# Kernel tuning notes

Measured on AMD Instinct MI355X. Metric: run time of the kernel, lower is better.

Reference implementation:

```python
import jax, jax.numpy as jnp
import numpy as np

L, B, N, D, H = 18, 2, 1024, 256, 4
DH = D // H  # head_dim = 64
LAYER_TYPES = ("self", "cross") * 9
BN_EPS = 1e-5


def setup_inputs() -> dict:
    key = jax.random.key(0)
    ks = jax.random.split(key, 8)
    s = 0.03  # small init scale keeps 18 residual layers numerically tame
    w = lambda k, shape: jax.random.normal(k, shape, jnp.float32) * s
    return dict(
        descriptors=jax.random.normal(ks[0], (B, 2, N, D), jnp.float32),
        mask=jnp.ones((B, 2, N), jnp.int32),
        qw=w(ks[1], (L, D, D)), qb=jnp.zeros((L, D), jnp.float32),
        kw=w(ks[2], (L, D, D)), kb=jnp.zeros((L, D), jnp.float32),
        vw=w(ks[3], (L, D, D)), vb=jnp.zeros((L, D), jnp.float32),
        ow=w(ks[4], (L, D, D)), ob=jnp.zeros((L, D), jnp.float32),
        w1=w(ks[5], (L, 2 * D, 2 * D)), b1=jnp.zeros((L, 2 * D), jnp.float32),
        bn_g=jnp.ones((L, 2 * D), jnp.float32), bn_b=jnp.zeros((L, 2 * D), jnp.float32),
        w2=w(ks[6], (L, 2 * D, D)), b2=jnp.zeros((L, D), jnp.float32),
    )


def _attention(x, src, m, i, qw, qb, kw, kb, vw, vb, ow, ob):
    b, n, d = x.shape
    q = (x @ qw[i] + qb[i]).reshape(b, n, H, DH)
    k = (src @ kw[i] + kb[i]).reshape(b, -1, H, DH)
    v = (src @ vw[i] + vb[i]).reshape(b, -1, H, DH)
    scores = jnp.einsum("bnhd,bmhd->bhnm", q, k) / (DH ** 0.5)
    scores = jnp.where(m[:, None, None, :] == 0, jnp.float32(-1e9), scores)
    probs = jax.nn.softmax(scores, axis=-1)  # fp32, matches torch dtype=float32
    out = jnp.einsum("bhnm,bmhd->bnhd", probs, v).reshape(b, n, d)
    return out @ ow[i] + ob[i]


def _propagate(x, src, m, i, qw, qb, kw, kb, vw, vb, ow, ob, w1, b1, bn_g, bn_b, w2, b2):
    a = _attention(x, src, m, i, qw, qb, kw, kb, vw, vb, ow, ob)
    h = jnp.concatenate([x, a], axis=-1)        # [B, N, 2D]
    h = h @ w1[i] + b1[i]                       # [B, N, 2D]
    # BatchNorm1d (training mode): per-channel stats over batch and keypoint dims
    mean = h.mean(axis=(0, 1))
    var = ((h - mean) ** 2).mean(axis=(0, 1))   # biased variance, as torch BN uses
    h = (h - mean) / jnp.sqrt(var + BN_EPS) * bn_g[i] + bn_b[i]
    h = jax.nn.relu(h)
    return h @ w2[i] + b2[i]                    # [B, N, D]


def reference(descriptors, mask, qw, qb, kw, kb, vw, vb, ow, ob, w1, b1, bn_g, bn_b, w2, b2):
    d0, d1 = descriptors[:, 0], descriptors[:, 1]
    m0, m1 = mask[:, 0], mask[:, 1]
    params = (qw, qb, kw, kb, vw, vb, ow, ob, w1, b1, bn_g, bn_b, w2, b2)
    for i, lt in enumerate(LAYER_TYPES):
        if lt == "cross":
            s0, s1, sm0, sm1 = d1, d0, m1, m0
        else:  # self
            s0, s1, sm0, sm1 = d0, d1, m0, m1
        delta0 = _propagate(d0, s0, sm0, i, *params)
        delta1 = _propagate(d1, s1, sm1, i, *params)
        d0 = d0 + delta0
        d1 = d1 + delta1
    return jnp.stack([d0, d1], axis=1)
```

## Files before the change

### kernel.cpp

```cpp
#include <hip/hip_runtime.h>


typedef __attribute__((ext_vector_type(8))) short bf16x8;
typedef __attribute__((ext_vector_type(4))) short bf16x4;
typedef __attribute__((ext_vector_type(4))) float floatx4;

__device__ __forceinline__ short f2b(float f) {
  unsigned u = __builtin_bit_cast(unsigned, f);
  unsigned r = (u + 0x7FFFu + ((u >> 16) & 1u)) >> 16;
  return (short)r;
}
__device__ __forceinline__ unsigned pack2(float a, float b) {
  return (unsigned)(unsigned short)f2b(a) | ((unsigned)(unsigned short)f2b(b) << 16);
}
__device__ __forceinline__ void split2(float a, float b, unsigned& h, unsigned& l) {
  unsigned short ha = (unsigned short)f2b(a), hb = (unsigned short)f2b(b);
  float fa = __builtin_bit_cast(float, (unsigned)ha << 16);
  float fb = __builtin_bit_cast(float, (unsigned)hb << 16);
  h = (unsigned)ha | ((unsigned)hb << 16);
  l = pack2(a - fa, b - fb);
}

__device__ __forceinline__ void gl2lds16(const void* g, void* l) {
  __builtin_amdgcn_global_load_lds(
      (const __attribute__((address_space(1))) unsigned*)g,
      (__attribute__((address_space(3))) unsigned*)l, 16, 0, 0);
}

__device__ __forceinline__ floatx4 mfma16_bf16(bf16x4 a, bf16x4 b, floatx4 c) {
#if __has_builtin(__builtin_amdgcn_mfma_f32_16x16x16_bf16)
  return __builtin_amdgcn_mfma_f32_16x16x16_bf16(a, b, c, 0, 0, 0);
#elif __has_builtin(__builtin_amdgcn_mfma_f32_16x16x16bf16_1k)
  return __builtin_amdgcn_mfma_f32_16x16x16bf16_1k(a, b, c, 0, 0, 0);
#else
  asm volatile("v_mfma_f32_16x16x16_bf16 %0, %1, %2, %0" : "+v"(c) : "v"(a), "v"(b));
  return c;
#endif
}

#define BARW   asm volatile("s_barrier" ::: "memory")
#define WAITV8 asm volatile("s_waitcnt vmcnt(8)" ::: "memory")
#define WAITV4 asm volatile("s_waitcnt vmcnt(4)" ::: "memory")
#define WAITV0 asm volatile("s_waitcnt vmcnt(0)" ::: "memory")
#define LGKM0  asm volatile("s_waitcnt lgkmcnt(0)" ::: "memory")
#define PRIO1  __builtin_amdgcn_s_setprio(1)
#define PRIO0  __builtin_amdgcn_s_setprio(0)

#define GEMM_IDS                                        \
  const int tid = threadIdx.x;                          \
  const int lane = tid & 63, w = tid >> 6;              \
  const int wy = w >> 1, wx = w & 1;                    \
  const int quad = lane >> 4, l16 = lane & 15;          \
  const int lr = lane >> 3;                             \
  const int lcs = (((lane & 7) ^ lr) & 7) * 8;          \
  const floatx4 z4 = {0.f, 0.f, 0.f, 0.f};

__device__ __forceinline__ void mfma_step_sw(const short* As, const short* Bs,
                                             int wy, int wx, int quad, int l16,
                                             floatx4 acc[2][4]) {
#pragma unroll
  for (int kk = 0; kk < 2; ++kk) {
    const int sw = (((kk * 4 + quad) ^ (l16 & 7)) * 8);
    bf16x8 a0 = *(const bf16x8*)&As[(wy * 32 + l16) * 64 + sw];
    bf16x8 a1 = *(const bf16x8*)&As[(wy * 32 + 16 + l16) * 64 + sw];
    bf16x8 b[4];
#pragma unroll
    for (int ni = 0; ni < 4; ++ni)
      b[ni] = *(const bf16x8*)&Bs[(wx * 64 + ni * 16 + l16) * 64 + sw];
#pragma unroll
    for (int ni = 0; ni < 4; ++ni) {
      acc[0][ni] = __builtin_amdgcn_mfma_f32_16x16x32_bf16(a0, b[ni], acc[0][ni], 0, 0, 0);
      acc[1][ni] = __builtin_amdgcn_mfma_f32_16x16x32_bf16(a1, b[ni], acc[1][ni], 0, 0, 0);
    }
  }
}

__device__ __forceinline__ void mfma_step_sw32(const short* As, const short* Bs,
                                               int wy, int wx, int quad, int l16,
                                               floatx4 acc[4]) {
#pragma unroll
  for (int kk = 0; kk < 2; ++kk) {
    const int sw = (((kk * 4 + quad) ^ (l16 & 7)) * 8);
    bf16x8 a0 = *(const bf16x8*)&As[(wy * 16 + l16) * 64 + sw];
    bf16x8 b[4];
#pragma unroll
    for (int ni = 0; ni < 4; ++ni)
      b[ni] = *(const bf16x8*)&Bs[(wx * 64 + ni * 16 + l16) * 64 + sw];
#pragma unroll
    for (int ni = 0; ni < 4; ++ni)
      acc[ni] = __builtin_amdgcn_mfma_f32_16x16x32_bf16(a0, b[ni], acc[ni], 0, 0, 0);
  }
}

__device__ __forceinline__ void mfma_step_sw32x64(const short* As, const short* Bs,
                                                  int wy, int wx, int quad, int l16,
                                                  floatx4 acc[2]) {
#pragma unroll
  for (int kk = 0; kk < 2; ++kk) {
    const int sw = (((kk * 4 + quad) ^ (l16 & 7)) * 8);
    bf16x8 a0 = *(const bf16x8*)&As[(wy * 16 + l16) * 64 + sw];
    bf16x8 b[2];
#pragma unroll
    for (int ni = 0; ni < 2; ++ni)
      b[ni] = *(const bf16x8*)&Bs[(wx * 32 + ni * 16 + l16) * 64 + sw];
#pragma unroll
    for (int ni = 0; ni < 2; ++ni)
      acc[ni] = __builtin_amdgcn_mfma_f32_16x16x32_bf16(a0, b[ni], acc[ni], 0, 0, 0);
  }
}

__global__ __launch_bounds__(256) void wfuse(
    const float* __restrict__ ow, const float* __restrict__ w1,
    short* __restrict__ wbuf) {
  __shared__ short As_h[64 * 64], As_l[64 * 64];
  __shared__ short Bs_h[128 * 64], Bs_l[128 * 64];
  const int blk = blockIdx.x;
  const int layer = blk >> 4, sub = blk & 15;
  const int kp0 = (sub & 3) * 64, n0 = (sub >> 2) * 128;
  const float* A = ow + (size_t)layer * 65536;
  const float* Bw = w1 + (size_t)layer * 262144 + 256 * 512;
  short* w1t = wbuf + (size_t)layer * 655360 + 262144;
  GEMM_IDS;
  (void)lr; (void)lcs;
  floatx4 acc[2][4] = {{z4, z4, z4, z4}, {z4, z4, z4, z4}};
  const int ar = tid >> 2, aq = tid & 3;
  const int bn = tid & 127, bkh = tid >> 7;

  for (int s = 0; s < 4; ++s) {
    const int k0 = s * 64;
    const float* Ar = &A[(size_t)(kp0 + ar) * 256 + k0 + aq * 16];
    float4 f0 = *(const float4*)&Ar[0];
    float4 f1 = *(const float4*)&Ar[4];
    float4 f2 = *(const float4*)&Ar[8];
    float4 f3 = *(const float4*)&Ar[12];
    float bv[32];
#pragma unroll
    for (int kk2 = 0; kk2 < 32; ++kk2)
      bv[kk2] = Bw[(size_t)(k0 + bkh * 32 + kk2) * 512 + n0 + bn];

    __syncthreads();
    {
      uint4 hi, lo;
      split2(f0.x, f0.y, hi.x, lo.x);
      split2(f0.z, f0.w, hi.y, lo.y);
      split2(f1.x, f1.y, hi.z, lo.z);
      split2(f1.z, f1.w, hi.w, lo.w);
      int sl = ((aq * 2) ^ (ar & 7)) * 8;
      *(uint4*)&As_h[ar * 64 + sl] = hi;
      *(uint4*)&As_l[ar * 64 + sl] = lo;
      split2(f2.x, f2.y, hi.x, lo.x);
      split2(f2.z, f2.w, hi.y, lo.y);
      split2(f3.x, f3.y, hi.z, lo.z);
      split2(f3.z, f3.w, hi.w, lo.w);
      sl = ((aq * 2 + 1) ^ (ar & 7)) * 8;
      *(uint4*)&As_h[ar * 64 + sl] = hi;
      *(uint4*)&As_l[ar * 64 + sl] = lo;
    }
#pragma unroll
    for (int cc = 0; cc < 4; ++cc) {
      uint4 hi, lo;
      split2(bv[cc * 8 + 0], bv[cc * 8 + 1], hi.x, lo.x);
      split2(bv[cc * 8 + 2], bv[cc * 8 + 3], hi.y, lo.y);
      split2(bv[cc * 8 + 4], bv[cc * 8 + 5], hi.z, lo.z);
      split2(bv[cc * 8 + 6], bv[cc * 8 + 7], hi.w, lo.w);
      int sl = ((bkh * 4 + cc) ^ (bn & 7)) * 8;
      *(uint4*)&Bs_h[bn * 64 + sl] = hi;
      *(uint4*)&Bs_l[bn * 64 + sl] = lo;
    }
    __syncthreads();
    mfma_step_sw(As_h, Bs_h, wy, wx, quad, l16, acc);
    mfma_step_sw(As_h, Bs_l, wy, wx, quad, l16, acc);
    mfma_step_sw(As_l, Bs_h, wy, wx, quad, l16, acc);
  }
#pragma unroll
  for (int mi = 0; mi < 2; ++mi)
#pragma unroll
    for (int ni = 0; ni < 4; ++ni) {
      int col = n0 + wx * 64 + ni * 16 + l16;
      int row0 = kp0 + wy * 32 + mi * 16 + quad * 4;
      uint2 uu;
      uu.x = pack2(acc[mi][ni][0], acc[mi][ni][1]);
      uu.y = pack2(acc[mi][ni][2], acc[mi][ni][3]);
      *(uint2*)&w1t[(size_t)col * 512 + 256 + row0] = uu;
    }
}

__global__ __launch_bounds__(256) void wprep(
    const float* __restrict__ qw, const float* __restrict__ kw,
    const float* __restrict__ vw, const float* __restrict__ w1,
    const float* __restrict__ w2, const float* __restrict__ ob,
    const float* __restrict__ b1, short* __restrict__ wbuf,
    float* __restrict__ beff, const float* __restrict__ desc,
    float* __restrict__ xd, short* __restrict__ xb,
    float* __restrict__ psz) {
  __shared__ float SH[32 * 130];
  int blk = blockIdx.x;
  int t = threadIdx.x;
  if (blk < 2592) {
    int layer = blk / 144;
    int sub2 = blk % 144;
    int sub = sub2 >> 1;
    int khalf = sub2 & 1;
    const float* W; int Kd, Nd, k0, n0; size_t ooff;
    if (sub < 24) {
      int wsel = sub / 8; int tt = sub & 7;
      k0 = (tt >> 1) * 64; n0 = (tt & 1) * 128; Kd = 256; Nd = 256;
      W = (wsel == 0 ? qw : wsel == 1 ? kw : vw) + (size_t)layer * 65536;
      ooff = (size_t)wsel * 65536;
    } else if (sub < 56) {
      int tt = sub - 24; k0 = (tt >> 2) * 64; n0 = (tt & 3) * 128;
      Kd = 512; Nd = 512; W = w1 + (size_t)layer * 262144; ooff = 262144;
    } else {
      int tt = sub - 56; k0 = (tt >> 1) * 64; n0 = (tt & 1) * 128;
      Kd = 512; Nd = 256; W = w2 + (size_t)layer * 131072; ooff = 524288;
    }
    k0 += khalf * 32;
    short* out = wbuf + (size_t)layer * 655360 + ooff;
    const int rr = t >> 4;
    const int c4 = (t & 15) * 4;
#pragma unroll
    for (int i = 0; i < 2; ++i)
#pragma unroll
      for (int hf = 0; hf < 2; ++hf) {
        float4 v = *(const float4*)&W[(size_t)(k0 + i * 16 + rr) * Nd + n0 + hf * 64 + c4];
        float* tp = &SH[(i * 16 + rr) * 130 + hf * 64 + c4];
        tp[0] = v.x; tp[1] = v.y; tp[2] = v.z; tp[3] = v.w;
      }
    __syncthreads();
    const int n = t >> 1;
    const int kh = (t & 1) * 16;
    float v[16];
#pragma unroll
    for (int kk = 0; kk < 16; ++kk)
      v[kk] = SH[(kh + kk) * 130 + n];
    unsigned u[8];
#pragma unroll
    for (int j2 = 0; j2 < 8; ++j2) u[j2] = pack2(v[2 * j2], v[2 * j2 + 1]);
    short* op = &out[(size_t)(n0 + n) * Kd + k0 + kh];
    uint4 o1; o1.x = u[0]; o1.y = u[1]; o1.z = u[2]; o1.w = u[3];
    uint4 o2; o2.x = u[4]; o2.y = u[5]; o2.z = u[6]; o2.w = u[7];
    *(uint4*)&op[0] = o1;
    *(uint4*)&op[8] = o2;
  } else if (blk < 2736) {
    int bb = blk - 2592;
    int layer = bb >> 3;
    int n0 = (bb & 7) * 64;
    const float* obL = ob + (size_t)layer * 256;
    const float* w1L = w1 + (size_t)layer * 262144 + 256 * 512;
    int n = n0 + (t & 63);
    int part = t >> 6;
    float s = 0.f;
    for (int i = part * 64; i < part * 64 + 64; ++i)
      s += obL[i] * w1L[(size_t)i * 512 + n];
    SH[part * 64 + (t & 63)] = s;
    __syncthreads();
    if (t < 64) {
      float tot = SH[t] + SH[64 + t] + SH[128 + t] + SH[192 + t] +
                  b1[(size_t)layer * 512 + n0 + t];
      beff[(size_t)layer * 512 + n0 + t] = tot;
    }
  } else if (blk < 3760) {
    int idx = (blk - 2736) * 256 + t;
    int fi = idx << 2;
    int hi = (fi >> 19) & 1;
    int lo = (fi >> 18) & 1;
    int sj = (fi & ~(3 << 18)) | (lo << 19) | (hi << 18);
    float4 v = *(const float4*)&desc[sj];
    *(float4*)&xd[fi] = v;
    uint2 uu; uu.x = pack2(v.x, v.y); uu.y = pack2(v.z, v.w);
    *(uint2*)&xb[fi] = uu;
  } else {
    int idx = (blk - 3760) * 1024 + t * 4;
    float4 zz = {0.f, 0.f, 0.f, 0.f};
    *(float4*)&psz[idx] = zz;
  }
}

__global__ __launch_bounds__(256, 2) void gemm_qkv(
    const short* __restrict__ xb, const short* __restrict__ wbufL,
    const float* __restrict__ qb_, const float* __restrict__ kb_,
    const float* __restrict__ vb_,
    short* __restrict__ q, short* __restrict__ kout, short* __restrict__ vT,
    int cross) {
  __shared__ short SM[40960];
  short* As = SM;
  short* Bs = SM + 8192;
  const int bid = blockIdx.x;
  const int swz = (bid & 7) * 96 + (bid >> 3);
  const int rb = (swz / 6) * 32;
  const int cb = (swz % 6) * 128;
  const int seg = cb >> 8;
  const int cbl = cb & 255;
  int arb = rb;
  if (seg) arb = (rb & 2047) | ((((rb >> 11) ^ cross) & 1) << 11);
  const short* A = xb + (size_t)arb * 256;
  const short* Wt = wbufL + (size_t)seg * 65536 + (size_t)cbl * 256;
  const float* bias = (seg == 0 ? qb_ : seg == 1 ? kb_ : vb_) + cbl;
  GEMM_IDS;
  floatx4 acc[4] = {z4, z4, z4, z4};

#pragma unroll
  for (int s = 0; s < 4; ++s) {
    const int k0 = s * 64;
    gl2lds16(&A[(size_t)(w * 8 + lr) * 256 + k0 + lcs], &As[s * 2048 + (w * 8) * 64]);
#pragma unroll
    for (int i = 0; i < 4; ++i)
      gl2lds16(&Wt[(size_t)(i * 32 + w * 8 + lr) * 256 + k0 + lcs],
               &Bs[s * 8192 + (i * 32 + w * 8) * 64]);
  }
  WAITV0;
  BARW;
#pragma unroll
  for (int s = 0; s < 4; ++s)
    mfma_step_sw32(&As[s * 2048], &Bs[s * 8192], wy, wx, quad, l16, acc);

  if (seg < 2) {
    short* C = (seg == 0 ? q : kout) + (size_t)rb * 256 + cbl;
#pragma unroll
    for (int ni = 0; ni < 4; ++ni) {
      int col = wx * 64 + ni * 16 + l16;
      float bc = bias[col];
#pragma unroll
      for (int reg = 0; reg < 4; ++reg) {
        int row = wy * 16 + quad * 4 + reg;
        C[(size_t)row * 256 + col] = f2b(acc[ni][reg] + bc);
      }
    }
  } else {
    BARW;
    short* T = SM + w * 1536;
    const int sb = rb >> 10;
    const int hh = (cbl >> 6) + wx;
    const int z = sb * 4 + hh;
#pragma unroll
    for (int ni = 0; ni < 4; ++ni) {
      int col = wx * 64 + ni * 16 + l16;
      float bc = bias[col];
#pragma unroll
      for (int reg = 0; reg < 4; ++reg)
        T[(ni * 16 + l16) * 24 + quad * 4 + reg] = f2b(acc[ni][reg] + bc);
    }
    short* dst = &vT[((size_t)z * 64 + lane) * 1024 + (rb & 1023) + wy * 16];
    *(uint4*)&dst[0] = *(const uint4*)&T[lane * 24 + 0];
    *(uint4*)&dst[8] = *(const uint4*)&T[lane * 24 + 8];
  }
}

__global__ __launch_bounds__(256, 3) void attn_mfma(
    const short* __restrict__ q, const short* __restrict__ k,
    const short* __restrict__ vT, const int* __restrict__ mask,
    short* __restrict__ attnb, int cross) {
  __shared__ short Ks[2][2][4096];
  __shared__ short Vs[2][4096];
  __shared__ float Msk[1024];
  const int tid = threadIdx.x;
  const int lane = tid & 63, w = tid >> 6;
  const int wv = w & 1, wq = w >> 1;
  const int quad = lane >> 4, l16 = lane & 15;
  const int lr = lane >> 3;
  const int lcs = (((lane & 7) ^ lr) & 7) * 8;
  const int bid = blockIdx.x;
  const int swz = (bid & 7) * 64 + (bid >> 3);
  const int qt = swz & 31;
  const int z = swz >> 5;
  const int sb = z >> 2, h = z & 3;
  const int s = sb >> 1, b = sb & 1;
  const int rowbase = sb * 1024;
  const int* mp = mask + (b * 2 + (s ^ cross)) * 1024;

  const int qrow = qt * 32 + wq * 16 + l16;
  bf16x8 qf[2];
#pragma unroll
  for (int kk = 0; kk < 2; ++kk)
    qf[kk] = *(const bf16x8*)&q[(size_t)(rowbase + qrow) * 256 + h * 64 + kk * 32 + quad * 8];

  {
    int4 mv = *(const int4*)&mp[tid * 4];
    Msk[tid * 4 + 0] = (mv.x == 0) ? -1.0e9f : 0.f;
    Msk[tid * 4 + 1] = (mv.y == 0) ? -1.0e9f : 0.f;
    Msk[tid * 4 + 2] = (mv.z == 0) ? -1.0e9f : 0.f;
    Msk[tid * 4 + 3] = (mv.w == 0) ? -1.0e9f : 0.f;
  }

  const floatx4 z4 = {0.f, 0.f, 0.f, 0.f};
  floatx4 o4[4] = {z4, z4, z4, z4};
  float mrun = -1e30f, lsum = 0.f;

#define ATT_STAGE_K(t, buf)                                                             \
  {                                                                                     \
    int key0s = wv * 512 + (t) * 64;                                                    \
    _Pragma("unroll") for (int j = 0; j < 4; ++j)                                       \
      gl2lds16(&k[(size_t)(rowbase + key0s + j * 16 + wq * 8 + lr) * 256 + h * 64 + lcs], \
               &Ks[buf][wv][(j * 16 + wq * 8) * 64]);                                   \
  }
#define ATT_STAGE_V(t)                                                                  \
  {                                                                                     \
    int key0s = wv * 512 + (t) * 64;                                                    \
    _Pragma("unroll") for (int j = 0; j < 4; ++j)                                       \
      gl2lds16(&vT[((size_t)z * 64 + j * 16 + wq * 8 + lr) * 1024 + key0s + lcs],       \
               &Vs[wv][(j * 16 + wq * 8) * 64]);                                        \
  }

  ATT_STAGE_K(0, 0);
  ATT_STAGE_V(0);
  __syncthreads();
  for (int t = 0; t < 8; ++t) {
    int buf = t & 1;
    if (t < 7) { ATT_STAGE_K(t + 1, buf ^ 1); WAITV8; } else { WAITV4; }
    BARW;
    const int key0 = wv * 512 + t * 64;

    floatx4 sA[4] = {z4, z4, z4, z4};
    PRIO1;
#pragma unroll
    for (int kk = 0; kk < 2; ++kk) {
      const int sw = (((kk * 4 + quad) ^ (l16 & 7)) * 8);
#pragma unroll
      for (int mt = 0; mt < 4; ++mt) {
        bf16x8 kf = *(const bf16x8*)&Ks[buf][wv][(mt * 16 + l16) * 64 + sw];
        sA[mt] = __builtin_amdgcn_mfma_f32_16x16x32_bf16(kf, qf[kk], sA[mt], 0, 0, 0);
      }
    }
    PRIO0;
    float scv[4][4];
    float tmax = -1e30f;
#pragma unroll
    for (int mt = 0; mt < 4; ++mt) {
      float4 mk = *(const float4*)&Msk[key0 + mt * 16 + quad * 4];
      scv[mt][0] = sA[mt][0] * 0.125f + mk.x;
      scv[mt][1] = sA[mt][1] * 0.125f + mk.y;
      scv[mt][2] = sA[mt][2] * 0.125f + mk.z;
      scv[mt][3] = sA[mt][3] * 0.125f + mk.w;
#pragma unroll
      for (int reg = 0; reg < 4; ++reg) tmax = fmaxf(tmax, scv[mt][reg]);
    }
    tmax = fmaxf(tmax, __shfl_xor(tmax, 16));
    tmax = fmaxf(tmax, __shfl_xor(tmax, 32));
    float mnew = fmaxf(mrun, tmax);
    float corr = __expf(mrun - mnew);
    mrun = mnew;
    lsum *= corr;
#pragma unroll
    for (int dt = 0; dt < 4; ++dt)
#pragma unroll
      for (int reg = 0; reg < 4; ++reg) o4[dt][reg] *= corr;

    bf16x4 pb[4];
#pragma unroll
    for (int mt = 0; mt < 4; ++mt) {
      float e0 = __expf(scv[mt][0] - mnew);
      float e1 = __expf(scv[mt][1] - mnew);
      float e2 = __expf(scv[mt][2] - mnew);
      float e3 = __expf(scv[mt][3] - mnew);
      lsum += (e0 + e1) + (e2 + e3);
      union { bf16x4 v; uint2 u; } pu;
      pu.u.x = pack2(e0, e1); pu.u.y = pack2(e2, e3);
      pb[mt] = pu.v;
    }
    if (t < 7) { WAITV4; } else { WAITV0; }
    BARW;
    PRIO1;
#pragma unroll
    for (int mt = 0; mt < 4; ++mt) {
      const int c2 = mt * 2 + (quad >> 1);
      const int sub = (quad & 1) * 4;
#pragma unroll
      for (int dt = 0; dt < 4; ++dt) {
        bf16x4 vf = *(const bf16x4*)&Vs[wv][(dt * 16 + l16) * 64 +
                                            ((c2 ^ (l16 & 7)) * 8) + sub];
        o4[dt] = mfma16_bf16(vf, pb[mt], o4[dt]);
      }
    }
    PRIO0;
    LGKM0;
    BARW;
    if (t < 7) ATT_STAGE_V(t + 1);
  }
  lsum += __shfl_xor(lsum, 16);
  lsum += __shfl_xor(lsum, 32);

  float* MG = (float*)&Ks[0][0][0];
  const int mo = (wq * 64 + lane) * 18;
  if (wv == 1) {
    MG[mo] = mrun;
    MG[mo + 1] = lsum;
#pragma unroll
    for (int dt = 0; dt < 4; ++dt)
#pragma unroll
      for (int reg = 0; reg < 4; ++reg) MG[mo + 2 + dt * 4 + reg] = o4[dt][reg];
  }
  __syncthreads();
  if (wv == 0) {
    float m2 = MG[mo], l2 = MG[mo + 1];
    float mm = fmaxf(mrun, m2);
    float ca = __expf(mrun - mm), cb2 = __expf(m2 - mm);
    float inv = 1.f / (ca * lsum + cb2 * l2);
    short* op = &attnb[(size_t)(rowbase + qrow) * 256 + h * 64 + quad * 4];
#pragma unroll
    for (int dt = 0; dt < 4; ++dt) {
      float v0 = (ca * o4[dt][0] + cb2 * MG[mo + 2 + dt * 4 + 0]) * inv;
      float v1 = (ca * o4[dt][1] + cb2 * MG[mo + 2 + dt * 4 + 1]) * inv;
      float v2 = (ca * o4[dt][2] + cb2 * MG[mo + 2 + dt * 4 + 2]) * inv;
      float v3 = (ca * o4[dt][3] + cb2 * MG[mo + 2 + dt * 4 + 3]) * inv;
      uint2 uu;
      uu.x = pack2(v0, v1);
      uu.y = pack2(v2, v3);
      *(uint2*)&op[dt * 16] = uu;
    }
  }
#undef ATT_STAGE_K
#undef ATT_STAGE_V
}

__global__ __launch_bounds__(256, 2) void gemm_w1(
    const short* __restrict__ xb, const short* __restrict__ attnb,
    const short* __restrict__ w1t, const float* __restrict__ beff,
    float* __restrict__ hbuf, float* __restrict__ psumL, float* __restrict__ psqL) {
  __shared__ short SM[40960];
  short* As = SM;
  short* Bs = SM + 8192;
  const int bid = blockIdx.x;
  const int swz = (bid & 7) * 64 + (bid >> 3);
  const int rb = (swz >> 2) * 32, cb = (swz & 3) * 128;
  const int str = rb >> 11;
  GEMM_IDS;
  floatx4 acc[4] = {z4, z4, z4, z4};

#pragma unroll
  for (int h = 0; h < 2; ++h) {
    if (h) BARW;
    const short* Ap = (h == 0 ? xb : attnb) + (size_t)rb * 256;
#pragma unroll
    for (int st = 0; st < 4; ++st) {
      const int k0 = h * 256 + st * 64;
      gl2lds16(&Ap[(size_t)(w * 8 + lr) * 256 + st * 64 + lcs],
               &As[st * 2048 + (w * 8) * 64]);
#pragma unroll
      for (int i = 0; i < 4; ++i)
        gl2lds16(&w1t[(size_t)(cb + i * 32 + w * 8 + lr) * 512 + k0 + lcs],
                 &Bs[st * 8192 + (i * 32 + w * 8) * 64]);
    }
    WAITV0;
    BARW;
#pragma unroll
    for (int st = 0; st < 4; ++st)
      mfma_step_sw32(&As[st * 2048], &Bs[st * 8192], wy, wx, quad, l16, acc);
  }

  float colsum[4], colsq[4];
#pragma unroll
  for (int ni = 0; ni < 4; ++ni) { colsum[ni] = 0.f; colsq[ni] = 0.f; }
#pragma unroll
  for (int ni = 0; ni < 4; ++ni) {
    int col = wx * 64 + ni * 16 + l16;
    float bc = beff[cb + col];
#pragma unroll
    for (int reg = 0; reg < 4; ++reg) {
      int row = rb + wy * 16 + quad * 4 + reg;
      float val = acc[ni][reg] + bc;
      hbuf[(size_t)row * 512 + cb + col] = val;
      colsum[ni] += val; colsq[ni] += val * val;
    }
  }
#pragma unroll
  for (int ni = 0; ni < 4; ++ni)
#pragma unroll
    for (int d = 16; d < 64; d <<= 1) {
      colsum[ni] += __shfl_xor(colsum[ni], d);
      colsq[ni]  += __shfl_xor(colsq[ni], d);
    }
  __syncthreads();
  float (*Ps)[2][128] = (float(*)[2][128])SM;
  if (quad == 0) {
#pragma unroll
    for (int ni = 0; ni < 4; ++ni) {
      Ps[wy][0][wx * 64 + ni * 16 + l16] = colsum[ni];
      Ps[wy][1][wx * 64 + ni * 16 + l16] = colsq[ni];
    }
  }
  __syncthreads();
  if (tid < 128) {
    atomicAdd(&psumL[str * 512 + cb + tid], Ps[0][0][tid] + Ps[1][0][tid]);
    atomicAdd(&psqL [str * 512 + cb + tid], Ps[0][1][tid] + Ps[1][1][tid]);
  }
}

__global__ __launch_bounds__(256, 3) void gemm_w2(
    const float* __restrict__ hbuf, const short* __restrict__ w2t,
    const float* __restrict__ b2_, const float* __restrict__ psumL,
    const float* __restrict__ psqL, const float* __restrict__ g,
    const float* __restrict__ be, float* __restrict__ xd, short* __restrict__ xb,
    float* __restrict__ outp) {
  __shared__ short SM[24576];
  __shared__ float s_scale[512], s_shift[512];
  short* As = SM;
  short* Bs = SM + 8192;
  const int bid = blockIdx.x;
  const int swz = (bid & 7) * 64 + (bid >> 3);
  const int rb = (swz >> 2) * 32, cb = (swz & 3) * 64;
  const int str = rb >> 11;
  GEMM_IDS;
  floatx4 acc[2] = {z4, z4};
#pragma unroll
  for (int cc = 0; cc < 2; ++cc) {
    int c = tid + cc * 256;
    float sum = psumL[str * 512 + c];
    float sq  = psqL [str * 512 + c];
    float mean = sum * (1.f / 2048.f);
    float var = sq * (1.f / 2048.f) - mean * mean;
    float rstd = rsqrtf(var + 1e-5f);
    float gs = g[c] * rstd;
    s_scale[c] = gs;
    s_shift[c] = be[c] - mean * gs;
  }
  __syncthreads();

  const int p = tid & 7, ar = tid >> 3;

#pragma unroll
  for (int h = 0; h < 2; ++h) {
    if (h) BARW;
#pragma unroll
    for (int st = 0; st < 4; ++st) {
      const int k0 = h * 256 + st * 64;
#pragma unroll
      for (int i = 0; i < 2; ++i)
        gl2lds16(&w2t[(size_t)(cb + i * 32 + w * 8 + lr) * 512 + k0 + lcs],
                 &Bs[st * 4096 + (i * 32 + w * 8) * 64]);
    }
#pragma unroll
    for (int st = 0; st < 4; ++st) {
      const int cs = h * 256 + st * 64 + ((p ^ (ar & 7)) * 8);
      float4 h0 = *(const float4*)&hbuf[(size_t)(rb + ar) * 512 + cs];
      float4 h1 = *(const float4*)&hbuf[(size_t)(rb + ar) * 512 + cs + 4];
      float4 sc0 = *(const float4*)&s_scale[cs];
      float4 sc1 = *(const float4*)&s_scale[cs + 4];
      float4 sh0 = *(const float4*)&s_shift[cs];
      float4 sh1 = *(const float4*)&s_shift[cs + 4];
      uint4 pk;
      pk.x = pack2(fmaxf(h0.x * sc0.x + sh0.x, 0.f), fmaxf(h0.y * sc0.y + sh0.y, 0.f));
      pk.y = pack2(fmaxf(h0.z * sc0.z + sh0.z, 0.f), fmaxf(h0.w * sc0.w + sh0.w, 0.f));
      pk.z = pack2(fmaxf(h1.x * sc1.x + sh1.x, 0.f), fmaxf(h1.y * sc1.y + sh1.y, 0.f));
      pk.w = pack2(fmaxf(h1.z * sc1.z + sh1.z, 0.f), fmaxf(h1.w * sc1.w + sh1.w, 0.f));
      *(uint4*)&As[st * 2048 + ar * 64 + p * 8] = pk;
    }
    WAITV0;
    LGKM0;
    BARW;
#pragma unroll
    for (int st = 0; st < 4; ++st)
      mfma_step_sw32x64(&As[st * 2048], &Bs[st * 4096], wy, wx, quad, l16, acc);
  }

#pragma unroll
  for (int ni = 0; ni < 2; ++ni) {
    int col = cb + wx * 32 + ni * 16 + l16;
    float bc = b2_[col];
#pragma unroll
    for (int reg = 0; reg < 4; ++reg) {
      int row = rb + wy * 16 + quad * 4 + reg;
      float r = xd[(size_t)row * 256 + col] + acc[ni][reg] + bc;
      xd[(size_t)row * 256 + col] = r;
      xb[(size_t)row * 256 + col] = f2b(r);
      if (outp) {
        int ss = row >> 11, bb = (row >> 10) & 1, n = row & 1023;
        outp[(size_t)((bb * 2 + ss) * 1024 + n) * 256 + col] = r;
      }
    }
  }
}

extern "C" void kernel_launch(void* const* d_in, const int* in_sizes, int n_in,
                              void* d_out, int out_size, void* d_ws, size_t ws_size,
                              hipStream_t stream) {
  (void)in_sizes; (void)n_in; (void)out_size; (void)ws_size;
  const float* desc = (const float*)d_in[0];
  const int*   mask = (const int*)d_in[1];
  const float* qw = (const float*)d_in[2];
  const float* qb = (const float*)d_in[3];
  const float* kw = (const float*)d_in[4];
  const float* kb = (const float*)d_in[5];
  const float* vw = (const float*)d_in[6];
  const float* vb = (const float*)d_in[7];
  const float* ow = (const float*)d_in[8];
  const float* ob = (const float*)d_in[9];
  const float* w1 = (const float*)d_in[10];
  const float* b1 = (const float*)d_in[11];
  const float* bn_g = (const float*)d_in[12];
  const float* bn_b = (const float*)d_in[13];
  const float* w2 = (const float*)d_in[14];
  const float* b2 = (const float*)d_in[15];
  float* out = (float*)d_out;

  char* base = (char*)d_ws;
  float* xd    = (float*)(base);
  float* hbuf  = (float*)(base + (4u << 20));
  short* xb    = (short*)(base + (12u << 20));
  short* qb16  = (short*)(base + (14u << 20));
  short* kb16  = (short*)(base + (16u << 20));
  short* vTb   = (short*)(base + (18u << 20));
  short* attnb = (short*)(base + (20u << 20));
  float* psum  = (float*)(base + (22u << 20));
  float* psq   = psum + 18 * 1024;
  float* beff  = psq + 18 * 1024;
  short* wbuf  = (short*)(base + (24u << 20));

  wprep<<<3796, 256, 0, stream>>>(qw, kw, vw, w1, w2, ob, b1,
                                  wbuf, beff, desc, xd, xb, psum);
  wfuse<<<288, 256, 0, stream>>>(ow, w1, wbuf);

  for (int i = 0; i < 18; ++i) {
    int cross = i & 1;
    short* wb = wbuf + (size_t)i * 655360;

    gemm_qkv<<<768, 256, 0, stream>>>(
        xb, wb, qb + (size_t)i * 256, kb + (size_t)i * 256, vb + (size_t)i * 256,
        qb16, kb16, vTb, cross);
    attn_mfma<<<512, 256, 0, stream>>>(qb16, kb16, vTb, mask, attnb, cross);
    gemm_w1<<<512, 256, 0, stream>>>(xb, attnb, wb + 262144,
                                     beff + (size_t)i * 512,
                                     hbuf, psum + (size_t)i * 1024,
                                     psq + (size_t)i * 1024);
    gemm_w2<<<512, 256, 0, stream>>>(hbuf, wb + 524288,
                                     b2 + (size_t)i * 256,
                                     psum + (size_t)i * 1024,
                                     psq + (size_t)i * 1024,
                                     bn_g + (size_t)i * 512,
                                     bn_b + (size_t)i * 512, xd, xb,
                                     (i == 17) ? out : nullptr);
  }
}
```

Before: 883.1 us.

## Double-buffer K-loop and double M-tile in QKV, W1, W2 GEMMs

The three projection GEMMs now use 64-row tiles instead of 32, halving the grid sizes. Each K loop changes from loading all stages and then computing into a two-buffer pipeline: global-to-LDS loads of stage s+2 (or s+1 in W2) are issued while stage s is multiplied. LDS use per block drops, so launch bounds rise to allow more resident blocks. The intent is to overlap memory latency with MFMA work and reuse each weight tile across more rows. The cost is fewer blocks on a GPU with many CUs, and extra barriers inside every K step.

```diff
diff --git a/kernel.cpp b/kernel.cpp
--- a/kernel.cpp
+++ b/kernel.cpp
@@ -40,6 +40,7 @@
 
 #define BARW   asm volatile("s_barrier" ::: "memory")
 #define WAITV8 asm volatile("s_waitcnt vmcnt(8)" ::: "memory")
+#define WAITV6 asm volatile("s_waitcnt vmcnt(6)" ::: "memory")
 #define WAITV4 asm volatile("s_waitcnt vmcnt(4)" ::: "memory")
 #define WAITV0 asm volatile("s_waitcnt vmcnt(0)" ::: "memory")
 #define LGKM0  asm volatile("s_waitcnt lgkmcnt(0)" ::: "memory")
@@ -75,37 +76,23 @@
   }
 }
 
-__device__ __forceinline__ void mfma_step_sw32(const short* As, const short* Bs,
+__device__ __forceinline__ void mfma_step_sw64(const short* As, const short* Bs,
                                                int wy, int wx, int quad, int l16,
-                                               floatx4 acc[4]) {
+                                               floatx4 acc[2][2]) {
 #pragma unroll
   for (int kk = 0; kk < 2; ++kk) {
     const int sw = (((kk * 4 + quad) ^ (l16 & 7)) * 8);
-    bf16x8 a0 = *(const bf16x8*)&As[(wy * 16 + l16) * 64 + sw];
-    bf16x8 b[4];
-#pragma unroll
-    for (int ni = 0; ni < 4; ++ni)
-      b[ni] = *(const bf16x8*)&Bs[(wx * 64 + ni * 16 + l16) * 64 + sw];
-#pragma unroll
-    for (int ni = 0; ni < 4; ++ni)
-      acc[ni] = __builtin_amdgcn_mfma_f32_16x16x32_bf16(a0, b[ni], acc[ni], 0, 0, 0);
-  }
-}
-
-__device__ __forceinline__ void mfma_step_sw32x64(const short* As, const short* Bs,
-                                                  int wy, int wx, int quad, int l16,
-                                                  floatx4 acc[2]) {
-#pragma unroll
-  for (int kk = 0; kk < 2; ++kk) {
-    const int sw = (((kk * 4 + quad) ^ (l16 & 7)) * 8);
-    bf16x8 a0 = *(const bf16x8*)&As[(wy * 16 + l16) * 64 + sw];
+    bf16x8 a0 = *(const bf16x8*)&As[(wy * 32 + l16) * 64 + sw];
+    bf16x8 a1 = *(const bf16x8*)&As[(wy * 32 + 16 + l16) * 64 + sw];
     bf16x8 b[2];
 #pragma unroll
     for (int ni = 0; ni < 2; ++ni)
       b[ni] = *(const bf16x8*)&Bs[(wx * 32 + ni * 16 + l16) * 64 + sw];
 #pragma unroll
-    for (int ni = 0; ni < 2; ++ni)
-      acc[ni] = __builtin_amdgcn_mfma_f32_16x16x32_bf16(a0, b[ni], acc[ni], 0, 0, 0);
+    for (int ni = 0; ni < 2; ++ni) {
+      acc[0][ni] = __builtin_amdgcn_mfma_f32_16x16x32_bf16(a0, b[ni], acc[0][ni], 0, 0, 0);
+      acc[1][ni] = __builtin_amdgcn_mfma_f32_16x16x32_bf16(a1, b[ni], acc[1][ni], 0, 0, 0);
+    }
   }
 }
 
@@ -276,18 +263,18 @@
   }
 }
 
-__global__ __launch_bounds__(256, 2) void gemm_qkv(
+__global__ __launch_bounds__(256, 3) void gemm_qkv(
     const short* __restrict__ xb, const short* __restrict__ wbufL,
     const float* __restrict__ qb_, const float* __restrict__ kb_,
     const float* __restrict__ vb_,
     short* __restrict__ q, short* __restrict__ kout, short* __restrict__ vT,
     int cross) {
-  __shared__ short SM[40960];
+  __shared__ short SM[2 * 4096 + 2 * 8192];
   short* As = SM;
   short* Bs = SM + 8192;
   const int bid = blockIdx.x;
-  const int swz = (bid & 7) * 96 + (bid >> 3);
-  const int rb = (swz / 6) * 32;
+  const int swz = (bid & 7) * 48 + (bid >> 3);
+  const int rb = (swz / 6) * 64;
   const int cb = (swz % 6) * 128;
   const int seg = cb >> 8;
   const int cbl = cb & 255;
@@ -297,53 +284,65 @@
   const short* Wt = wbufL + (size_t)seg * 65536 + (size_t)cbl * 256;
   const float* bias = (seg == 0 ? qb_ : seg == 1 ? kb_ : vb_) + cbl;
   GEMM_IDS;
-  floatx4 acc[4] = {z4, z4, z4, z4};
-
-#pragma unroll
+  floatx4 acc[2][4] = {{z4, z4, z4, z4}, {z4, z4, z4, z4}};
+
+#define QKV_STAGE(s, buf)                                                          \
+  {                                                                                \
+    int k0 = (s) * 64;                                                             \
+    gl2lds16(&A[(size_t)(w * 8 + lr) * 256 + k0 + lcs], &As[(buf) * 4096 + (w * 8) * 64]); \
+    gl2lds16(&A[(size_t)(32 + w * 8 + lr) * 256 + k0 + lcs], &As[(buf) * 4096 + (32 + w * 8) * 64]); \
+    _Pragma("unroll") for (int i = 0; i < 4; ++i)                                  \
+      gl2lds16(&Wt[(size_t)(i * 32 + w * 8 + lr) * 256 + k0 + lcs],                \
+               &Bs[(buf) * 8192 + (i * 32 + w * 8) * 64]);                         \
+  }
+
+  QKV_STAGE(0, 0);
+  QKV_STAGE(1, 1);
   for (int s = 0; s < 4; ++s) {
-    const int k0 = s * 64;
-    gl2lds16(&A[(size_t)(w * 8 + lr) * 256 + k0 + lcs], &As[s * 2048 + (w * 8) * 64]);
-#pragma unroll
-    for (int i = 0; i < 4; ++i)
-      gl2lds16(&Wt[(size_t)(i * 32 + w * 8 + lr) * 256 + k0 + lcs],
-               &Bs[s * 8192 + (i * 32 + w * 8) * 64]);
-  }
-  WAITV0;
-  BARW;
-#pragma unroll
-  for (int s = 0; s < 4; ++s)
-    mfma_step_sw32(&As[s * 2048], &Bs[s * 8192], wy, wx, quad, l16, acc);
+    int buf = s & 1;
+    if (s < 3) { WAITV6; } else { WAITV0; }
+    BARW;
+    mfma_step_sw(&As[buf * 4096], &Bs[buf * 8192], wy, wx, quad, l16, acc);
+    BARW;
+    if (s < 2) QKV_STAGE(s + 2, buf);
+  }
 
   if (seg < 2) {
     short* C = (seg == 0 ? q : kout) + (size_t)rb * 256 + cbl;
 #pragma unroll
-    for (int ni = 0; ni < 4; ++ni) {
-      int col = wx * 64 + ni * 16 + l16;
-      float bc = bias[col];
-#pragma unroll
-      for (int reg = 0; reg < 4; ++reg) {
-        int row = wy * 16 + quad * 4 + reg;
-        C[(size_t)row * 256 + col] = f2b(acc[ni][reg] + bc);
+    for (int mi = 0; mi < 2; ++mi)
+#pragma unroll
+      for (int ni = 0; ni < 4; ++ni) {
+        int col = wx * 64 + ni * 16 + l16;
+        float bc = bias[col];
+#pragma unroll
+        for (int reg = 0; reg < 4; ++reg) {
+          int row = wy * 32 + mi * 16 + quad * 4 + reg;
+          C[(size_t)row * 256 + col] = f2b(acc[mi][ni][reg] + bc);
+        }
       }
-    }
   } else {
-    BARW;
-    short* T = SM + w * 1536;
+    short* T = SM + w * 2560;
     const int sb = rb >> 10;
     const int hh = (cbl >> 6) + wx;
     const int z = sb * 4 + hh;
 #pragma unroll
-    for (int ni = 0; ni < 4; ++ni) {
-      int col = wx * 64 + ni * 16 + l16;
-      float bc = bias[col];
-#pragma unroll
-      for (int reg = 0; reg < 4; ++reg)
-        T[(ni * 16 + l16) * 24 + quad * 4 + reg] = f2b(acc[ni][reg] + bc);
-    }
-    short* dst = &vT[((size_t)z * 64 + lane) * 1024 + (rb & 1023) + wy * 16];
-    *(uint4*)&dst[0] = *(const uint4*)&T[lane * 24 + 0];
-    *(uint4*)&dst[8] = *(const uint4*)&T[lane * 24 + 8];
-  }
+    for (int mi = 0; mi < 2; ++mi)
+#pragma unroll
+      for (int ni = 0; ni < 4; ++ni) {
+        int col = wx * 64 + ni * 16 + l16;
+        float bc = bias[col];
+#pragma unroll
+        for (int reg = 0; reg < 4; ++reg)
+          T[(ni * 16 + l16) * 40 + mi * 16 + quad * 4 + reg] =
+              f2b(acc[mi][ni][reg] + bc);
+      }
+    short* dst = &vT[((size_t)z * 64 + lane) * 1024 + (rb & 1023) + wy * 32];
+#pragma unroll
+    for (int c = 0; c < 4; ++c)
+      *(uint4*)&dst[c * 8] = *(const uint4*)&T[lane * 40 + c * 8];
+  }
+#undef QKV_STAGE
 }
 
 __global__ __launch_bounds__(256, 3) void attn_mfma(
@@ -512,56 +511,60 @@
 #undef ATT_STAGE_V
 }
 
-__global__ __launch_bounds__(256, 2) void gemm_w1(
+__global__ __launch_bounds__(256, 3) void gemm_w1(
     const short* __restrict__ xb, const short* __restrict__ attnb,
     const short* __restrict__ w1t, const float* __restrict__ beff,
     float* __restrict__ hbuf, float* __restrict__ psumL, float* __restrict__ psqL) {
-  __shared__ short SM[40960];
+  __shared__ short SM[2 * 4096 + 2 * 8192];
+  __shared__ float Ps[2][2][128];
   short* As = SM;
   short* Bs = SM + 8192;
   const int bid = blockIdx.x;
-  const int swz = (bid & 7) * 64 + (bid >> 3);
-  const int rb = (swz >> 2) * 32, cb = (swz & 3) * 128;
+  const int swz = (bid & 7) * 32 + (bid >> 3);
+  const int rb = (swz >> 2) * 64, cb = (swz & 3) * 128;
   const int str = rb >> 11;
   GEMM_IDS;
-  floatx4 acc[4] = {z4, z4, z4, z4};
-
-#pragma unroll
-  for (int h = 0; h < 2; ++h) {
-    if (h) BARW;
-    const short* Ap = (h == 0 ? xb : attnb) + (size_t)rb * 256;
-#pragma unroll
-    for (int st = 0; st < 4; ++st) {
-      const int k0 = h * 256 + st * 64;
-      gl2lds16(&Ap[(size_t)(w * 8 + lr) * 256 + st * 64 + lcs],
-               &As[st * 2048 + (w * 8) * 64]);
-#pragma unroll
-      for (int i = 0; i < 4; ++i)
-        gl2lds16(&w1t[(size_t)(cb + i * 32 + w * 8 + lr) * 512 + k0 + lcs],
-                 &Bs[st * 8192 + (i * 32 + w * 8) * 64]);
-    }
-    WAITV0;
-    BARW;
-#pragma unroll
-    for (int st = 0; st < 4; ++st)
-      mfma_step_sw32(&As[st * 2048], &Bs[st * 8192], wy, wx, quad, l16, acc);
-  }
-
+  floatx4 acc[2][4] = {{z4, z4, z4, z4}, {z4, z4, z4, z4}};
+
+#define W1_STAGE(s, buf)                                                            \
+  {                                                                                 \
+    int k0 = (s) * 64;                                                              \
+    const short* Ap = ((s) < 4 ? xb : attnb) + (size_t)rb * 256;                    \
+    int kb = k0 & 255;                                                              \
+    gl2lds16(&Ap[(size_t)(w * 8 + lr) * 256 + kb + lcs], &As[(buf) * 4096 + (w * 8) * 64]); \
+    gl2lds16(&Ap[(size_t)(32 + w * 8 + lr) * 256 + kb + lcs], &As[(buf) * 4096 + (32 + w * 8) * 64]); \
+    _Pragma("unroll") for (int i = 0; i < 4; ++i)                                   \
+      gl2lds16(&w1t[(size_t)(cb + i * 32 + w * 8 + lr) * 512 + k0 + lcs],           \
+               &Bs[(buf) * 8192 + (i * 32 + w * 8) * 64]);                          \
+  }
+
+  W1_STAGE(0, 0);
+  W1_STAGE(1, 1);
+  for (int s = 0; s < 8; ++s) {
+    int buf = s & 1;
+    if (s < 7) { WAITV6; } else { WAITV0; }
+    BARW;
+    mfma_step_sw(&As[buf * 4096], &Bs[buf * 8192], wy, wx, quad, l16, acc);
+    BARW;
+    if (s < 6) W1_STAGE(s + 2, buf);
+  }
   float colsum[4], colsq[4];
 #pragma unroll
   for (int ni = 0; ni < 4; ++ni) { colsum[ni] = 0.f; colsq[ni] = 0.f; }
 #pragma unroll
-  for (int ni = 0; ni < 4; ++ni) {
-    int col = wx * 64 + ni * 16 + l16;
-    float bc = beff[cb + col];
-#pragma unroll
-    for (int reg = 0; reg < 4; ++reg) {
-      int row = rb + wy * 16 + quad * 4 + reg;
-      float val = acc[ni][reg] + bc;
-      hbuf[(size_t)row * 512 + cb + col] = val;
-      colsum[ni] += val; colsq[ni] += val * val;
-    }
-  }
+  for (int mi = 0; mi < 2; ++mi)
+#pragma unroll
+    for (int ni = 0; ni < 4; ++ni) {
+      int col = wx * 64 + ni * 16 + l16;
+      float bc = beff[cb + col];
+#pragma unroll
+      for (int reg = 0; reg < 4; ++reg) {
+        int row = rb + wy * 32 + mi * 16 + quad * 4 + reg;
+        float val = acc[mi][ni][reg] + bc;
+        hbuf[(size_t)row * 512 + cb + col] = val;
+        colsum[ni] += val; colsq[ni] += val * val;
+      }
+    }
 #pragma unroll
   for (int ni = 0; ni < 4; ++ni)
 #pragma unroll
@@ -569,8 +572,6 @@
       colsum[ni] += __shfl_xor(colsum[ni], d);
       colsq[ni]  += __shfl_xor(colsq[ni], d);
     }
-  __syncthreads();
-  float (*Ps)[2][128] = (float(*)[2][128])SM;
   if (quad == 0) {
 #pragma unroll
     for (int ni = 0; ni < 4; ++ni) {
@@ -583,24 +584,25 @@
     atomicAdd(&psumL[str * 512 + cb + tid], Ps[0][0][tid] + Ps[1][0][tid]);
     atomicAdd(&psqL [str * 512 + cb + tid], Ps[0][1][tid] + Ps[1][1][tid]);
   }
-}
-
-__global__ __launch_bounds__(256, 3) void gemm_w2(
+#undef W1_STAGE
+}
+
+__global__ __launch_bounds__(256, 4) void gemm_w2(
     const float* __restrict__ hbuf, const short* __restrict__ w2t,
     const float* __restrict__ b2_, const float* __restrict__ psumL,
     const float* __restrict__ psqL, const float* __restrict__ g,
     const float* __restrict__ be, float* __restrict__ xd, short* __restrict__ xb,
     float* __restrict__ outp) {
-  __shared__ short SM[24576];
+  __shared__ short SM[2 * 4096 + 2 * 4096];
   __shared__ float s_scale[512], s_shift[512];
   short* As = SM;
   short* Bs = SM + 8192;
   const int bid = blockIdx.x;
-  const int swz = (bid & 7) * 64 + (bid >> 3);
-  const int rb = (swz >> 2) * 32, cb = (swz & 3) * 64;
+  const int swz = (bid & 7) * 32 + (bid >> 3);
+  const int rb = (swz >> 2) * 64, cb = (swz & 3) * 64;
   const int str = rb >> 11;
   GEMM_IDS;
-  floatx4 acc[2] = {z4, z4};
+  floatx4 acc[2][2] = {{z4, z4}, {z4, z4}};
 #pragma unroll
   for (int cc = 0; cc < 2; ++cc) {
     int c = tid + cc * 256;
@@ -616,58 +618,85 @@
   __syncthreads();
 
   const int p = tid & 7, ar = tid >> 3;
-
-#pragma unroll
-  for (int h = 0; h < 2; ++h) {
-    if (h) BARW;
-#pragma unroll
-    for (int st = 0; st < 4; ++st) {
-      const int k0 = h * 256 + st * 64;
-#pragma unroll
-      for (int i = 0; i < 2; ++i)
-        gl2lds16(&w2t[(size_t)(cb + i * 32 + w * 8 + lr) * 512 + k0 + lcs],
-                 &Bs[st * 4096 + (i * 32 + w * 8) * 64]);
-    }
-#pragma unroll
-    for (int st = 0; st < 4; ++st) {
-      const int cs = h * 256 + st * 64 + ((p ^ (ar & 7)) * 8);
-      float4 h0 = *(const float4*)&hbuf[(size_t)(rb + ar) * 512 + cs];
-      float4 h1 = *(const float4*)&hbuf[(size_t)(rb + ar) * 512 + cs + 4];
-      float4 sc0 = *(const float4*)&s_scale[cs];
-      float4 sc1 = *(const float4*)&s_scale[cs + 4];
-      float4 sh0 = *(const float4*)&s_shift[cs];
-      float4 sh1 = *(const float4*)&s_shift[cs + 4];
-      uint4 pk;
-      pk.x = pack2(fmaxf(h0.x * sc0.x + sh0.x, 0.f), fmaxf(h0.y * sc0.y + sh0.y, 0.f));
-      pk.y = pack2(fmaxf(h0.z * sc0.z + sh0.z, 0.f), fmaxf(h0.w * sc0.w + sh0.w, 0.f));
-      pk.z = pack2(fmaxf(h1.x * sc1.x + sh1.x, 0.f), fmaxf(h1.y * sc1.y + sh1.y, 0.f));
-      pk.w = pack2(fmaxf(h1.z * sc1.z + sh1.z, 0.f), fmaxf(h1.w * sc1.w + sh1.w, 0.f));
-      *(uint4*)&As[st * 2048 + ar * 64 + p * 8] = pk;
-    }
-    WAITV0;
+  float4 ra0, ra1, ra2, ra3;
+
+#define W2_A_LOAD(s)                                                               \
+  {                                                                                \
+    int k0 = (s) * 64;                                                             \
+    int cs0 = k0 + ((p ^ (ar & 7)) * 8);                                           \
+    int cs1 = k0 + ((p ^ ((ar + 32) & 7)) * 8);                                    \
+    ra0 = *(const float4*)&hbuf[(size_t)(rb + ar) * 512 + cs0];                    \
+    ra1 = *(const float4*)&hbuf[(size_t)(rb + ar) * 512 + cs0 + 4];                \
+    ra2 = *(const float4*)&hbuf[(size_t)(rb + 32 + ar) * 512 + cs1];               \
+    ra3 = *(const float4*)&hbuf[(size_t)(rb + 32 + ar) * 512 + cs1 + 4];           \
+  }
+#define W2_A_WRITE(s, buf)                                                         \
+  {                                                                                \
+    int k0 = (s) * 64;                                                             \
+    int cs0 = k0 + ((p ^ (ar & 7)) * 8);                                           \
+    int cs1 = k0 + ((p ^ ((ar + 32) & 7)) * 8);                                    \
+    float4 sc0 = *(const float4*)&s_scale[cs0];                                    \
+    float4 sc1 = *(const float4*)&s_scale[cs0 + 4];                                \
+    float4 sh0 = *(const float4*)&s_shift[cs0];                                    \
+    float4 sh1 = *(const float4*)&s_shift[cs0 + 4];                                \
+    uint4 pk;                                                                      \
+    pk.x = pack2(fmaxf(ra0.x * sc0.x + sh0.x, 0.f), fmaxf(ra0.y * sc0.y + sh0.y, 0.f)); \
+    pk.y = pack2(fmaxf(ra0.z * sc0.z + sh0.z, 0.f), fmaxf(ra0.w * sc0.w + sh0.w, 0.f)); \
+    pk.z = pack2(fmaxf(ra1.x * sc1.x + sh1.x, 0.f), fmaxf(ra1.y * sc1.y + sh1.y, 0.f)); \
+    pk.w = pack2(fmaxf(ra1.z * sc1.z + sh1.z, 0.f), fmaxf(ra1.w * sc1.w + sh1.w, 0.f)); \
+    *(uint4*)&As[(buf) * 4096 + ar * 64 + p * 8] = pk;                             \
+    float4 sc2 = *(const float4*)&s_scale[cs1];                                    \
+    float4 sc3 = *(const float4*)&s_scale[cs1 + 4];                                \
+    float4 sh2 = *(const float4*)&s_shift[cs1];                                    \
+    float4 sh3 = *(const float4*)&s_shift[cs1 + 4];                                \
+    pk.x = pack2(fmaxf(ra2.x * sc2.x + sh2.x, 0.f), fmaxf(ra2.y * sc2.y + sh2.y, 0.f)); \
+    pk.y = pack2(fmaxf(ra2.z * sc2.z + sh2.z, 0.f), fmaxf(ra2.w * sc2.w + sh2.w, 0.f)); \
+    pk.z = pack2(fmaxf(ra3.x * sc3.x + sh3.x, 0.f), fmaxf(ra3.y * sc3.y + sh3.y, 0.f)); \
+    pk.w = pack2(fmaxf(ra3.z * sc3.z + sh3.z, 0.f), fmaxf(ra3.w * sc3.w + sh3.w, 0.f)); \
+    *(uint4*)&As[(buf) * 4096 + (32 + ar) * 64 + p * 8] = pk;                      \
+  }
+#define W2_STAGE_B(s, buf)                                                         \
+  {                                                                                \
+    int k0 = (s) * 64;                                                             \
+    _Pragma("unroll") for (int i = 0; i < 2; ++i)                                  \
+      gl2lds16(&w2t[(size_t)(cb + i * 32 + w * 8 + lr) * 512 + k0 + lcs],          \
+               &Bs[(buf) * 4096 + (i * 32 + w * 8) * 64]);                         \
+  }
+
+  W2_A_LOAD(0);
+  W2_STAGE_B(0, 0);
+  W2_A_WRITE(0, 0);
+  LGKM0;
+  for (int s = 0; s < 8; ++s) {
+    int buf = s & 1;
+    if (s < 7) { W2_A_LOAD(s + 1); W2_STAGE_B(s + 1, buf ^ 1); WAITV6; } else { WAITV0; }
+    BARW;
+    mfma_step_sw64(&As[buf * 4096], &Bs[buf * 4096], wy, wx, quad, l16, acc);
+    if (s < 7) W2_A_WRITE(s + 1, buf ^ 1);
     LGKM0;
     BARW;
-#pragma unroll
-    for (int st = 0; st < 4; ++st)
-      mfma_step_sw32x64(&As[st * 2048], &Bs[st * 4096], wy, wx, quad, l16, acc);
-  }
-
-#pragma unroll
-  for (int ni = 0; ni < 2; ++ni) {
-    int col = cb + wx * 32 + ni * 16 + l16;
-    float bc = b2_[col];
-#pragma unroll
-    for (int reg = 0; reg < 4; ++reg) {
-      int row = rb + wy * 16 + quad * 4 + reg;
-      float r = xd[(size_t)row * 256 + col] + acc[ni][reg] + bc;
-      xd[(size_t)row * 256 + col] = r;
-      xb[(size_t)row * 256 + col] = f2b(r);
-      if (outp) {
-        int ss = row >> 11, bb = (row >> 10) & 1, n = row & 1023;
-        outp[(size_t)((bb * 2 + ss) * 1024 + n) * 256 + col] = r;
+  }
+#pragma unroll
+  for (int mi = 0; mi < 2; ++mi)
+#pragma unroll
+    for (int ni = 0; ni < 2; ++ni) {
+      int col = cb + wx * 32 + ni * 16 + l16;
+      float bc = b2_[col];
+#pragma unroll
+      for (int reg = 0; reg < 4; ++reg) {
+        int row = rb + wy * 32 + mi * 16 + quad * 4 + reg;
+        float r = xd[(size_t)row * 256 + col] + acc[mi][ni][reg] + bc;
+        xd[(size_t)row * 256 + col] = r;
+        xb[(size_t)row * 256 + col] = f2b(r);
+        if (outp) {
+          int ss = row >> 11, bb = (row >> 10) & 1, n = row & 1023;
+          outp[(size_t)((bb * 2 + ss) * 1024 + n) * 256 + col] = r;
+        }
       }
     }
-  }
+#undef W2_A_LOAD
+#undef W2_A_WRITE
+#undef W2_STAGE_B
 }
 
 extern "C" void kernel_launch(void* const* d_in, const int* in_sizes, int n_in,
@@ -713,15 +742,15 @@
     int cross = i & 1;
     short* wb = wbuf + (size_t)i * 655360;
 
-    gemm_qkv<<<768, 256, 0, stream>>>(
+    gemm_qkv<<<384, 256, 0, stream>>>(
         xb, wb, qb + (size_t)i * 256, kb + (size_t)i * 256, vb + (size_t)i * 256,
         qb16, kb16, vTb, cross);
     attn_mfma<<<512, 256, 0, stream>>>(qb16, kb16, vTb, mask, attnb, cross);
-    gemm_w1<<<512, 256, 0, stream>>>(xb, attnb, wb + 262144,
+    gemm_w1<<<256, 256, 0, stream>>>(xb, attnb, wb + 262144,
                                      beff + (size_t)i * 512,
                                      hbuf, psum + (size_t)i * 1024,
                                      psq + (size_t)i * 1024);
-    gemm_w2<<<512, 256, 0, stream>>>(hbuf, wb + 524288,
+    gemm_w2<<<256, 256, 0, stream>>>(hbuf, wb + 524288,
                                      b2 + (size_t)i * 256,
                                      psum + (size_t)i * 1024,
                                      psq + (size_t)i * 1024,
```

Result: slower. 939.2 us (+6.3%).
